# Kernel tuning notes

Measured on AMD Instinct MI355X. Metric: run time of the kernel, lower is better.

## Reference

```python
import jax, jax.numpy as jnp
import numpy as np

TEMPERATURE = 0.1
THR = 0.2
BORDER_RM = 2


def setup_inputs() -> dict:
    key = jax.random.key(0)
    k0, k1 = jax.random.split(key)
    N, L, S, C = 2, 4800, 4800, 256
    return {
        "feat_c0": jax.random.normal(k0, (N, L, C), dtype=jnp.float32),
        "feat_c1": jax.random.normal(k1, (N, S, C), dtype=jnp.float32),
        "h0c": 60, "w0c": 80, "h1c": 60, "w1c": 80,
    }


def _border_valid(h, w, bd):
    # Faithful to torch mask_border: only the FIRST `bd` rows/cols are masked
    # (the negative slices m[:, -bd:0] in the source are empty no-ops).
    vh = jnp.arange(h) >= bd
    vw = jnp.arange(w) >= bd
    return (vh[:, None] & vw[None, :]).reshape(-1)  # [h*w]


def reference(feat_c0, feat_c1, h0c, w0c, h1c, w1c):
    C = feat_c0.shape[-1]
    scale = 1.0 / (C ** 0.5)  # 'sqrt_feat_dim' feature normalizer
    f0 = feat_c0 * scale
    f1 = feat_c1 * scale

    # dual-softmax confidence matrix [N, L, S]
    sim = jnp.einsum("nlc,nsc->nls", f0, f1) / TEMPERATURE
    conf = jax.nn.softmax(sim, axis=1) * jax.nn.softmax(sim, axis=2)

    # threshold + border removal (no padding masks in data)
    mask = conf > THR
    valid0 = _border_valid(h0c, w0c, BORDER_RM)  # [L]
    valid1 = _border_valid(h1c, w1c, BORDER_RM)  # [S]
    mask = mask & valid0[None, :, None] & valid1[None, None, :]

    # mutual nearest neighbour filtering
    mask = mask & (conf == conf.max(axis=2, keepdims=True)) \
                & (conf == conf.max(axis=1, keepdims=True))

    # match extraction (JIT-friendly padded form):
    # j_ids[b, i] = column of the (unique) True in row i; match_mask marks valid rows.
    j_ids = jnp.argmax(mask, axis=2)               # [N, L] int
    match_mask = jnp.any(mask, axis=2)             # [N, L] bool
    mconf = jnp.take_along_axis(conf, j_ids[..., None], axis=2)[..., 0]
    mconf = jnp.where(match_mask, mconf, 0.0)      # [N, L]

    return conf, match_mask, j_ids, mconf
```

## Files before the change

kernel.cpp:

```cpp
#include <hip/hip_runtime.h>


#define Ncst 2
#define Lc 4800
#define Sc 4800
#define Cc 256
#define K3 768
#define LP 4864
#define THRC 0.2f

typedef float f32x4 __attribute__((ext_vector_type(4)));
typedef __bf16 bf16x8 __attribute__((ext_vector_type(8)));

#define AS1(p) ((__attribute__((address_space(1))) void*)(p))
#define AS3(p) ((__attribute__((address_space(3))) void*)(p))

__device__ inline unsigned short f2bf(float x) {
    unsigned u = __float_as_uint(x);
    unsigned r = (u + 0x7fffu + ((u >> 16) & 1u)) >> 16;
    return (unsigned short)r;
}
__device__ inline float bf2f(unsigned short h) {
    return __uint_as_float(((unsigned)h) << 16);
}

__global__ __launch_bounds__(256) void init_kernel(float* __restrict__ rs, float* __restrict__ cs)
{
    int i = blockIdx.x * 256 + threadIdx.x;
    if (i < Ncst * Lc) { rs[i] = 0.f; cs[i] = 0.f; }
}

__global__ __launch_bounds__(256) void convert_kernel(
    const float* __restrict__ f0, const float* __restrict__ f1,
    unsigned short* __restrict__ A3, unsigned short* __restrict__ B3)
{
    int idx = blockIdx.x * 256 + threadIdx.x;
    if (idx >= Ncst * LP * (Cc / 8)) return;
    int k8  = idx & (Cc / 8 - 1);
    int row = (idx >> 5) % LP;
    int n   = idx / (LP * (Cc / 8));
    size_t base = ((size_t)n * LP + row) * K3 + k8 * 8;

    float av[8], bv[8];
    if (row < Lc) {
        const float4* pa = (const float4*)(f0 + ((size_t)n * Lc + row) * Cc + k8 * 8);
        float4 a0 = pa[0], a1 = pa[1];
        av[0]=a0.x; av[1]=a0.y; av[2]=a0.z; av[3]=a0.w;
        av[4]=a1.x; av[5]=a1.y; av[6]=a1.z; av[7]=a1.w;
        const float4* pb = (const float4*)(f1 + ((size_t)n * Sc + row) * Cc + k8 * 8);
        float4 b0 = pb[0], b1 = pb[1];
        bv[0]=b0.x; bv[1]=b0.y; bv[2]=b0.z; bv[3]=b0.w;
        bv[4]=b1.x; bv[5]=b1.y; bv[6]=b1.z; bv[7]=b1.w;
    } else {
        for (int i = 0; i < 8; ++i) { av[i] = 0.f; bv[i] = 0.f; }
    }

    unsigned short ahi[8], alo[8], bhi[8], blo[8];
#pragma unroll
    for (int i = 0; i < 8; ++i) {
        ahi[i] = f2bf(av[i]); alo[i] = f2bf(av[i] - bf2f(ahi[i]));
        bhi[i] = f2bf(bv[i]); blo[i] = f2bf(bv[i] - bf2f(bhi[i]));
    }
    *(uint4*)&A3[base]       = *(uint4*)ahi;
    *(uint4*)&A3[base + 256] = *(uint4*)ahi;
    *(uint4*)&A3[base + 512] = *(uint4*)alo;
    *(uint4*)&B3[base]       = *(uint4*)bhi;
    *(uint4*)&B3[base + 256] = *(uint4*)blo;
    *(uint4*)&B3[base + 512] = *(uint4*)bhi;
}

__global__ __launch_bounds__(256) void gemm_kernel(
    const unsigned short* __restrict__ A3, const unsigned short* __restrict__ B3,
    float* __restrict__ eout, float* __restrict__ rs, float* __restrict__ cs)
{
    __shared__ unsigned short lA[128 * 32];
    __shared__ unsigned short lB[128 * 32];

    const int n    = blockIdx.z;
    const int tm   = blockIdx.y;
    const int tn   = blockIdx.x;
    const int tid  = threadIdx.x;
    const int wave = tid >> 6;
    const int lane = tid & 63;
    const int wm   = wave >> 1;
    const int wn   = wave & 1;
    const int ml   = lane & 15;
    const int kq   = lane >> 4;

    const unsigned short* Ab = A3 + ((size_t)n * LP + (size_t)tm * 128) * K3;
    const unsigned short* Bb = B3 + ((size_t)n * LP + (size_t)tn * 128) * K3;

    f32x4 acc[4][4] = {};

    for (int k0 = 0; k0 < K3; k0 += 32) {
        __syncthreads();
#pragma unroll
        for (int cc = 0; cc < 2; ++cc) {
            int c    = wave * 2 + cc;
            int slot = c * 64 + lane;
            int row  = slot >> 2;
            int q    = (slot & 3) ^ ((row >> 1) & 3);
            const unsigned short* ga = Ab + (size_t)row * K3 + (k0 + q * 8);
            const unsigned short* gb = Bb + (size_t)row * K3 + (k0 + q * 8);
            __builtin_amdgcn_global_load_lds(AS1(ga), AS3(lA + (size_t)slot * 8), 16, 0, 0);
            __builtin_amdgcn_global_load_lds(AS1(gb), AS3(lB + (size_t)slot * 8), 16, 0, 0);
        }
        __syncthreads();

        bf16x8 af[4], bfr[4];
#pragma unroll
        for (int i = 0; i < 4; ++i) {
            int arow = wm * 64 + i * 16 + ml;
            int aslot = arow * 4 + (kq ^ ((arow >> 1) & 3));
            af[i] = *(const bf16x8*)&lA[aslot * 8];
            int brow = wn * 64 + i * 16 + ml;
            int bslot = brow * 4 + (kq ^ ((brow >> 1) & 3));
            bfr[i] = *(const bf16x8*)&lB[bslot * 8];
        }
#pragma unroll
        for (int i = 0; i < 4; ++i)
#pragma unroll
            for (int j = 0; j < 4; ++j)
                acc[i][j] = __builtin_amdgcn_mfma_f32_16x16x32_bf16(af[i], bfr[j], acc[i][j], 0, 0, 0);
    }

    const float alpha = 5.0f / 128.0f;
#pragma unroll
    for (int i = 0; i < 4; ++i) {
#pragma unroll
        for (int r = 0; r < 4; ++r) {
            int gl = tm * 128 + wm * 64 + i * 16 + kq * 4 + r;
            bool rok = gl < Lc;
#pragma unroll
            for (int j = 0; j < 4; ++j) {
                int gs = tn * 128 + wn * 64 + j * 16 + ml;
                bool ok = rok && (gs < Sc);
                float ev = ok ? __expf(acc[i][j][r] * alpha) : 0.f;
                acc[i][j][r] = ev;
                if (ok) eout[((size_t)n * Lc + gl) * Sc + gs] = ev;
            }
        }
    }
#pragma unroll
    for (int i = 0; i < 4; ++i) {
#pragma unroll
        for (int r = 0; r < 4; ++r) {
            float rp = acc[i][0][r] + acc[i][1][r] + acc[i][2][r] + acc[i][3][r];
            rp += __shfl_xor(rp, 1);
            rp += __shfl_xor(rp, 2);
            rp += __shfl_xor(rp, 4);
            rp += __shfl_xor(rp, 8);
            int gl = tm * 128 + wm * 64 + i * 16 + kq * 4 + r;
            if (ml == 0 && gl < Lc) atomicAdd(&rs[(size_t)n * Lc + gl], rp);
        }
    }
#pragma unroll
    for (int j = 0; j < 4; ++j) {
        float cp = 0.f;
#pragma unroll
        for (int i = 0; i < 4; ++i)
#pragma unroll
            for (int r = 0; r < 4; ++r) cp += acc[i][j][r];
        cp += __shfl_xor(cp, 16);
        cp += __shfl_xor(cp, 32);
        int gs = tn * 128 + wn * 64 + j * 16 + ml;
        if (kq == 0 && gs < Sc) atomicAdd(&cs[(size_t)n * Sc + gs], cp);
    }
}

__global__ __launch_bounds__(256) void inv_kernel(
    const float* __restrict__ rs, const float* __restrict__ cs,
    float* __restrict__ rsinv, float* __restrict__ csinv)
{
    int i = blockIdx.x * 256 + threadIdx.x;
    if (i < Ncst * Lc) { rsinv[i] = 1.0f / rs[i]; csinv[i] = 1.0f / cs[i]; }
}

__global__ __launch_bounds__(256) void conf_kernel(
    float* __restrict__ confio,
    const float* __restrict__ rsinv, const float* __restrict__ csinv,
    float* __restrict__ rcm)
{
    __shared__ float sh[256];
    int b = blockIdx.x;
    int n = b / Lc;
    f32x4* row = (f32x4*)(confio + (size_t)b * Sc);
    const f32x4* civ = (const f32x4*)(csinv + (size_t)n * Sc);
    int tid = threadIdx.x;
    float riv = rsinv[b];
    float lmax = 0.f;
    for (int v = tid; v < Sc / 4; v += 256) {
        f32x4 e4 = row[v];
        f32x4 c4 = civ[v];
        f32x4 o  = e4 * e4 * riv * c4;
        row[v] = o;
        lmax = fmaxf(lmax, fmaxf(fmaxf(o.x, o.y), fmaxf(o.z, o.w)));
    }
    sh[tid] = lmax;
    __syncthreads();
    for (int off = 128; off; off >>= 1) {
        if (tid < off) sh[tid] = fmaxf(sh[tid], sh[tid + off]);
        __syncthreads();
    }
    if (tid == 0) rcm[b] = sh[0];
}

__global__ __launch_bounds__(256) void finalize_kernel(
    const float* __restrict__ conf, const float* __restrict__ rcm,
    const int* __restrict__ h0p, const int* __restrict__ w0p,
    const int* __restrict__ h1p, const int* __restrict__ w1p,
    float* __restrict__ out_match, float* __restrict__ out_j, float* __restrict__ out_mconf)
{
    int i = blockIdx.x * 256 + threadIdx.x;
    if (i >= Ncst * Lc) return;
    int n = i / Lc, l = i % Lc;
    float mm = rcm[i];
    float fm = 0.f, fj = 0.f, fc = 0.f;
    if (mm > THRC) {
        int w0 = *w0p, w1 = *w1p;
        if ((l / w0) >= 2 && (l % w0) >= 2) {
            const float* rowp = conf + ((size_t)n * Lc + l) * Sc;
            for (int s = 0; s < Sc; ++s) {
                float c = rowp[s];
                if (c == mm && (s / w1) >= 2 && (s % w1) >= 2) {
                    bool ismax = true;
                    const float* colp = conf + (size_t)n * Lc * Sc + s;
                    for (int lp = 0; lp < Lc; ++lp) {
                        if (colp[(size_t)lp * Sc] > c) { ismax = false; break; }
                    }
                    if (ismax) { fm = 1.f; fj = (float)s; fc = c; break; }
                }
            }
        }
    }
    out_match[i] = fm; out_j[i] = fj; out_mconf[i] = fc;
}

extern "C" void kernel_launch(void* const* d_in, const int* in_sizes, int n_in,
                              void* d_out, int out_size, void* d_ws, size_t ws_size,
                              hipStream_t stream) {
    const float* f0 = (const float*)d_in[0];
    const float* f1 = (const float*)d_in[1];
    const int* h0p = (const int*)d_in[2];
    const int* w0p = (const int*)d_in[3];
    const int* h1p = (const int*)d_in[4];
    const int* w1p = (const int*)d_in[5];

    char* ws = (char*)d_ws;
    unsigned short* A3 = (unsigned short*)ws;
    unsigned short* B3 = (unsigned short*)(ws + 14942208);
    float* rs    = (float*)(ws + 29884416);
    float* cs    = (float*)(ws + 29922816);
    float* rsinv = (float*)(ws + 29961216);
    float* csinv = (float*)(ws + 29999616);
    float* rcm   = (float*)(ws + 30038016);

    float* conf      = (float*)d_out;
    float* out_match = conf + (size_t)Ncst * Lc * Sc;
    float* out_j     = out_match + Ncst * Lc;
    float* out_mconf = out_j + Ncst * Lc;

    init_kernel<<<(Ncst * Lc + 255) / 256, 256, 0, stream>>>(rs, cs);

    convert_kernel<<<(Ncst * LP * (Cc / 8) + 255) / 256, 256, 0, stream>>>(f0, f1, A3, B3);

    dim3 gg(LP / 128, LP / 128, Ncst);
    gemm_kernel<<<gg, 256, 0, stream>>>(A3, B3, conf, rs, cs);

    inv_kernel<<<(Ncst * Lc + 255) / 256, 256, 0, stream>>>(rs, cs, rsinv, csinv);

    conf_kernel<<<Ncst * Lc, 256, 0, stream>>>(conf, rsinv, csinv, rcm);

    finalize_kernel<<<(Ncst * Lc + 255) / 256, 256, 0, stream>>>(
        conf, rcm, h0p, w0p, h1p, w1p, out_match, out_j, out_mconf);
}
```

Before: 360.9 us.

## Switch split-precision GEMM from 3-term bf16 to 2-term fp16 with XCD swizzle

```diff
diff --git a/kernel.cpp b/kernel.cpp
--- a/kernel.cpp
+++ b/kernel.cpp
@@ -5,25 +5,16 @@
 #define Lc 4800
 #define Sc 4800
 #define Cc 256
-#define K3 768
+#define K2 512
 #define LP 4864
 #define THRC 0.2f
 
 typedef float f32x4 __attribute__((ext_vector_type(4)));
-typedef __bf16 bf16x8 __attribute__((ext_vector_type(8)));
+typedef _Float16 f16x8 __attribute__((ext_vector_type(8)));
 
 #define AS1(p) ((__attribute__((address_space(1))) void*)(p))
 #define AS3(p) ((__attribute__((address_space(3))) void*)(p))
 
-__device__ inline unsigned short f2bf(float x) {
-    unsigned u = __float_as_uint(x);
-    unsigned r = (u + 0x7fffu + ((u >> 16) & 1u)) >> 16;
-    return (unsigned short)r;
-}
-__device__ inline float bf2f(unsigned short h) {
-    return __uint_as_float(((unsigned)h) << 16);
-}
-
 __global__ __launch_bounds__(256) void init_kernel(float* __restrict__ rs, float* __restrict__ cs)
 {
     int i = blockIdx.x * 256 + threadIdx.x;
@@ -32,14 +23,14 @@
 
 __global__ __launch_bounds__(256) void convert_kernel(
     const float* __restrict__ f0, const float* __restrict__ f1,
-    unsigned short* __restrict__ A3, unsigned short* __restrict__ B3)
+    unsigned short* __restrict__ A2, unsigned short* __restrict__ B2)
 {
     int idx = blockIdx.x * 256 + threadIdx.x;
     if (idx >= Ncst * LP * (Cc / 8)) return;
     int k8  = idx & (Cc / 8 - 1);
     int row = (idx >> 5) % LP;
     int n   = idx / (LP * (Cc / 8));
-    size_t base = ((size_t)n * LP + row) * K3 + k8 * 8;
+    size_t base = ((size_t)n * LP + row) * K2 + k8 * 8;
 
     float av[8], bv[8];
     if (row < Lc) {
@@ -55,30 +46,33 @@
         for (int i = 0; i < 8; ++i) { av[i] = 0.f; bv[i] = 0.f; }
     }
 
-    unsigned short ahi[8], alo[8], bhi[8], blo[8];
+    _Float16 ahi[8], alo[8], bhi[8];
 #pragma unroll
     for (int i = 0; i < 8; ++i) {
-        ahi[i] = f2bf(av[i]); alo[i] = f2bf(av[i] - bf2f(ahi[i]));
-        bhi[i] = f2bf(bv[i]); blo[i] = f2bf(bv[i] - bf2f(bhi[i]));
-    }
-    *(uint4*)&A3[base]       = *(uint4*)ahi;
-    *(uint4*)&A3[base + 256] = *(uint4*)ahi;
-    *(uint4*)&A3[base + 512] = *(uint4*)alo;
-    *(uint4*)&B3[base]       = *(uint4*)bhi;
-    *(uint4*)&B3[base + 256] = *(uint4*)blo;
-    *(uint4*)&B3[base + 512] = *(uint4*)bhi;
+        _Float16 h = (_Float16)av[i];
+        ahi[i] = h;
+        alo[i] = (_Float16)(av[i] - (float)h);
+        bhi[i] = (_Float16)bv[i];
+    }
+    *(uint4*)&A2[base]       = *(uint4*)ahi;
+    *(uint4*)&A2[base + 256] = *(uint4*)alo;
+    *(uint4*)&B2[base]       = *(uint4*)bhi;
+    *(uint4*)&B2[base + 256] = *(uint4*)bhi;
 }
 
 __global__ __launch_bounds__(256) void gemm_kernel(
-    const unsigned short* __restrict__ A3, const unsigned short* __restrict__ B3,
+    const unsigned short* __restrict__ A2, const unsigned short* __restrict__ B2,
     float* __restrict__ eout, float* __restrict__ rs, float* __restrict__ cs)
 {
-    __shared__ unsigned short lA[128 * 32];
-    __shared__ unsigned short lB[128 * 32];
-
-    const int n    = blockIdx.z;
-    const int tm   = blockIdx.y;
-    const int tn   = blockIdx.x;
+    __shared__ unsigned short lA[128 * 64];
+    __shared__ unsigned short lB[128 * 64];
+
+    int flat = blockIdx.x + 38 * blockIdx.y + 1444 * blockIdx.z;
+    int m    = (flat & 7) * 361 + (flat >> 3);
+    const int tn = m % 38;
+    const int tm = (m / 38) % 38;
+    const int n  = m / 1444;
+
     const int tid  = threadIdx.x;
     const int wave = tid >> 6;
     const int lane = tid & 63;
@@ -87,41 +81,43 @@
     const int ml   = lane & 15;
     const int kq   = lane >> 4;
 
-    const unsigned short* Ab = A3 + ((size_t)n * LP + (size_t)tm * 128) * K3;
-    const unsigned short* Bb = B3 + ((size_t)n * LP + (size_t)tn * 128) * K3;
+    const unsigned short* Ab = A2 + ((size_t)n * LP + (size_t)tm * 128) * K2;
+    const unsigned short* Bb = B2 + ((size_t)n * LP + (size_t)tn * 128) * K2;
 
     f32x4 acc[4][4] = {};
 
-    for (int k0 = 0; k0 < K3; k0 += 32) {
+    for (int k0 = 0; k0 < K2; k0 += 64) {
         __syncthreads();
 #pragma unroll
-        for (int cc = 0; cc < 2; ++cc) {
-            int c    = wave * 2 + cc;
-            int slot = c * 64 + lane;
-            int row  = slot >> 2;
-            int q    = (slot & 3) ^ ((row >> 1) & 3);
-            const unsigned short* ga = Ab + (size_t)row * K3 + (k0 + q * 8);
-            const unsigned short* gb = Bb + (size_t)row * K3 + (k0 + q * 8);
+        for (int cc = 0; cc < 4; ++cc) {
+            int slot = (wave * 4 + cc) * 64 + lane;
+            int row  = slot >> 3;
+            int q    = (slot & 7) ^ (row & 7);
+            const unsigned short* ga = Ab + (size_t)row * K2 + (k0 + q * 8);
+            const unsigned short* gb = Bb + (size_t)row * K2 + (k0 + q * 8);
             __builtin_amdgcn_global_load_lds(AS1(ga), AS3(lA + (size_t)slot * 8), 16, 0, 0);
             __builtin_amdgcn_global_load_lds(AS1(gb), AS3(lB + (size_t)slot * 8), 16, 0, 0);
         }
         __syncthreads();
 
-        bf16x8 af[4], bfr[4];
-#pragma unroll
-        for (int i = 0; i < 4; ++i) {
-            int arow = wm * 64 + i * 16 + ml;
-            int aslot = arow * 4 + (kq ^ ((arow >> 1) & 3));
-            af[i] = *(const bf16x8*)&lA[aslot * 8];
-            int brow = wn * 64 + i * 16 + ml;
-            int bslot = brow * 4 + (kq ^ ((brow >> 1) & 3));
-            bfr[i] = *(const bf16x8*)&lB[bslot * 8];
-        }
-#pragma unroll
-        for (int i = 0; i < 4; ++i)
-#pragma unroll
-            for (int j = 0; j < 4; ++j)
-                acc[i][j] = __builtin_amdgcn_mfma_f32_16x16x32_bf16(af[i], bfr[j], acc[i][j], 0, 0, 0);
+#pragma unroll
+        for (int s = 0; s < 2; ++s) {
+            f16x8 af[4], bfr[4];
+#pragma unroll
+            for (int i = 0; i < 4; ++i) {
+                int arow = wm * 64 + i * 16 + ml;
+                int aq   = (s * 4 + kq) ^ (arow & 7);
+                af[i] = *(const f16x8*)&lA[((size_t)arow * 8 + aq) * 8];
+                int brow = wn * 64 + i * 16 + ml;
+                int bq   = (s * 4 + kq) ^ (brow & 7);
+                bfr[i] = *(const f16x8*)&lB[((size_t)brow * 8 + bq) * 8];
+            }
+#pragma unroll
+            for (int i = 0; i < 4; ++i)
+#pragma unroll
+                for (int j = 0; j < 4; ++j)
+                    acc[i][j] = __builtin_amdgcn_mfma_f32_16x16x32_f16(af[i], bfr[j], acc[i][j], 0, 0, 0);
+        }
     }
 
     const float alpha = 5.0f / 128.0f;
@@ -181,7 +177,7 @@
     const float* __restrict__ rsinv, const float* __restrict__ csinv,
     float* __restrict__ rcm)
 {
-    __shared__ float sh[256];
+    __shared__ float sw[4];
     int b = blockIdx.x;
     int n = b / Lc;
     f32x4* row = (f32x4*)(confio + (size_t)b * Sc);
@@ -196,13 +192,11 @@
         row[v] = o;
         lmax = fmaxf(lmax, fmaxf(fmaxf(o.x, o.y), fmaxf(o.z, o.w)));
     }
-    sh[tid] = lmax;
+#pragma unroll
+    for (int off = 1; off < 64; off <<= 1) lmax = fmaxf(lmax, __shfl_xor(lmax, off));
+    if ((tid & 63) == 0) sw[tid >> 6] = lmax;
     __syncthreads();
-    for (int off = 128; off; off >>= 1) {
-        if (tid < off) sh[tid] = fmaxf(sh[tid], sh[tid + off]);
-        __syncthreads();
-    }
-    if (tid == 0) rcm[b] = sh[0];
+    if (tid == 0) rcm[b] = fmaxf(fmaxf(sw[0], sw[1]), fmaxf(sw[2], sw[3]));
 }
 
 __global__ __launch_bounds__(256) void finalize_kernel(
@@ -247,13 +241,13 @@
     const int* w1p = (const int*)d_in[5];
 
     char* ws = (char*)d_ws;
-    unsigned short* A3 = (unsigned short*)ws;
-    unsigned short* B3 = (unsigned short*)(ws + 14942208);
-    float* rs    = (float*)(ws + 29884416);
-    float* cs    = (float*)(ws + 29922816);
-    float* rsinv = (float*)(ws + 29961216);
-    float* csinv = (float*)(ws + 29999616);
-    float* rcm   = (float*)(ws + 30038016);
+    unsigned short* A2 = (unsigned short*)ws;
+    unsigned short* B2 = (unsigned short*)(ws + 9961472);
+    float* rs    = (float*)(ws + 19922944);
+    float* cs    = (float*)(ws + 19961344);
+    float* rsinv = (float*)(ws + 19999744);
+    float* csinv = (float*)(ws + 20038144);
+    float* rcm   = (float*)(ws + 20076544);
 
     float* conf      = (float*)d_out;
     float* out_match = conf + (size_t)Ncst * Lc * Sc;
@@ -262,10 +256,10 @@
 
     init_kernel<<<(Ncst * Lc + 255) / 256, 256, 0, stream>>>(rs, cs);
 
-    convert_kernel<<<(Ncst * LP * (Cc / 8) + 255) / 256, 256, 0, stream>>>(f0, f1, A3, B3);
+    convert_kernel<<<(Ncst * LP * (Cc / 8) + 255) / 256, 256, 0, stream>>>(f0, f1, A2, B2);
 
     dim3 gg(LP / 128, LP / 128, Ncst);
-    gemm_kernel<<<gg, 256, 0, stream>>>(A3, B3, conf, rs, cs);
+    gemm_kernel<<<gg, 256, 0, stream>>>(A2, B2, conf, rs, cs);
 
     inv_kernel<<<(Ncst * Lc + 255) / 256, 256, 0, stream>>>(rs, cs, rsinv, csinv);
 
```

Measured after the change: 337.8 us. -6.4%, faster.
